# Kernel tuning notes

Measured on AMD Instinct MI355X. Metric: run time of the kernel, lower is better.

The kernel has to match this reference:

```python
import jax, jax.numpy as jnp
import numpy as np

N_NODES = 50000
N_EDGES = 1600000
IN_CH = 128
HID = 64
HEADS = 2
EMB = 128
OUT_CH = EMB // HEADS  # 64, GATConvMean out_channels
NEG_SLOPE = 0.2


def _gat_conv(x, src, dst, W, a_src, a_dst, b, heads, out_ch, concat, n_nodes):
    # x: [N, F_in]; W: [F_in, heads*out_ch]; a_src/a_dst: [heads, out_ch]; b: bias
    s = (x @ W).reshape(n_nodes, heads, out_ch)          # [N, H, C]
    alpha_src = jnp.sum(s * a_src, axis=-1)              # [N, H]
    alpha_dst = jnp.sum(s * a_dst, axis=-1)              # [N, H]
    e = jax.nn.leaky_relu(alpha_src[src] + alpha_dst[dst], NEG_SLOPE)  # [E, H]
    # segment softmax over edges sharing the same destination node
    m = jax.ops.segment_max(e, dst, num_segments=n_nodes)             # [N, H]
    ex = jnp.exp(e - m[dst])
    denom = jax.ops.segment_sum(ex, dst, num_segments=n_nodes)        # [N, H]
    alpha = ex / denom[dst]                                           # [E, H]
    msg = s[src] * alpha[:, :, None]                                  # [E, H, C]
    out = jax.ops.segment_sum(msg, dst, num_segments=n_nodes)         # [N, H, C]
    if concat:
        out = out.reshape(n_nodes, heads * out_ch)
    else:
        out = out.mean(axis=1)
    return out + b


def setup_inputs() -> dict:
    key = jax.random.key(0)
    ks = jax.random.split(key, 16)
    X = jax.random.normal(ks[0], (N_NODES, IN_CH), dtype=jnp.float32)
    edge_index = jax.random.randint(ks[1], (2, N_EDGES), 0, N_NODES, dtype=jnp.int64)

    def glorot(k, shape):
        fan_in, fan_out = shape[0], shape[-1]
        lim = jnp.sqrt(6.0 / (fan_in + fan_out)).astype(jnp.float32)
        return jax.random.uniform(k, shape, jnp.float32, -lim, lim)

    HC = HEADS * HID  # 128
    # in_layer: GATConv(IN_CH -> HID, heads=HEADS, concat)
    W0 = glorot(ks[2], (IN_CH, HC))
    a_src0 = glorot(ks[3], (HEADS, HID))
    a_dst0 = glorot(ks[4], (HEADS, HID))
    b0 = jnp.zeros((HC,), jnp.float32)
    # middle layer: GATConv(HC -> HID, heads=HEADS, concat)
    W1 = glorot(ks[5], (HC, HC))
    a_src1 = glorot(ks[6], (HEADS, HID))
    a_dst1 = glorot(ks[7], (HEADS, HID))
    b1 = jnp.zeros((HC,), jnp.float32)
    # ivectors: GATConvMean(HC -> OUT_CH, heads=HEADS, mean over heads)
    W2 = glorot(ks[8], (HC, HEADS * OUT_CH))
    a_src2 = glorot(ks[9], (HEADS, OUT_CH))
    a_dst2 = glorot(ks[10], (HEADS, OUT_CH))
    b2 = jnp.zeros((OUT_CH,), jnp.float32)
    return {
        "X": X, "edge_index": edge_index,
        "W0": W0, "a_src0": a_src0, "a_dst0": a_dst0, "b0": b0,
        "W1": W1, "a_src1": a_src1, "a_dst1": a_dst1, "b1": b1,
        "W2": W2, "a_src2": a_src2, "a_dst2": a_dst2, "b2": b2,
    }


def reference(X, edge_index, W0, a_src0, a_dst0, b0, W1, a_src1, a_dst1, b1, W2, a_src2, a_dst2, b2):
    n = X.shape[0]
    loop = jnp.arange(n, dtype=edge_index.dtype)
    src = jnp.concatenate([edge_index[0], loop])  # PyG GATConv add_self_loops=True
    dst = jnp.concatenate([edge_index[1], loop])
    h = jax.nn.elu(_gat_conv(X, src, dst, W0, a_src0, a_dst0, b0, HEADS, HID, True, n))
    h = jax.nn.relu(_gat_conv(h, src, dst, W1, a_src1, a_dst1, b1, HEADS, HID, True, n))
    # dropout is identity in eval mode
    out = jax.nn.relu(_gat_conv(h, src, dst, W2, a_src2, a_dst2, b2, HEADS, OUT_CH, False, n))
    return out
```

## Files before the change

### kernel.cpp

```cpp
#include <hip/hip_runtime.h>
#include <hip/hip_bf16.h>


#define SCAN_BLOCK 256

__global__ void detect_i64(const unsigned* __restrict__ ei, int* __restrict__ flag) {
    if (threadIdx.x == 0 && blockIdx.x == 0) {
        int allz = 1;
        for (int i = 0; i < 128; ++i)
            if (ei[2 * i + 1] != 0u) { allz = 0; break; }
        *flag = allz;
    }
}

__global__ __launch_bounds__(256) void gat_convert(
    const void* __restrict__ ei, const int* __restrict__ flag, int nE, int nN,
    int* __restrict__ srci, int* __restrict__ dsti) {
    const int i64 = *flag;
    const long long total = (long long)nE + nN;
    const long long stride = (long long)gridDim.x * blockDim.x;
    for (long long i = (long long)blockIdx.x * blockDim.x + threadIdx.x; i < total; i += stride) {
        int s, d;
        if (i < nE) {
            if (i64) { s = (int)((const long long*)ei)[i]; d = (int)((const long long*)ei)[nE + i]; }
            else     { s = ((const int*)ei)[i];            d = ((const int*)ei)[nE + i]; }
        } else { s = d = (int)(i - nE); }
        srci[i] = s;
        dsti[i] = d;
    }
}

__global__ __launch_bounds__(256) void gat_rankp(
    const int* __restrict__ dsti, long long total, int nN,
    int* __restrict__ cnt, int* __restrict__ rank) {
    const int cw = (nN + 7) >> 3;
    const int lo = (blockIdx.x & 7) * cw;
    const long long stride = (long long)(gridDim.x >> 3) * blockDim.x;
    for (long long i = (long long)(blockIdx.x >> 3) * blockDim.x + threadIdx.x;
         i < total; i += stride) {
        const int d = dsti[i];
        if ((unsigned)(d - lo) >= (unsigned)cw) continue;
        rank[i] = atomicAdd(&cnt[d], 1);
    }
}

__global__ __launch_bounds__(SCAN_BLOCK) void scan_stage1(
    const int* __restrict__ cnt, int* __restrict__ partial, int* __restrict__ bsum, int n) {
    __shared__ int tmp[SCAN_BLOCK];
    const int i = blockIdx.x * SCAN_BLOCK + threadIdx.x;
    const int v = (i < n) ? cnt[i] : 0;
    tmp[threadIdx.x] = v;
    __syncthreads();
    #pragma unroll
    for (int off = 1; off < SCAN_BLOCK; off <<= 1) {
        const int t = (threadIdx.x >= off) ? tmp[threadIdx.x - off] : 0;
        __syncthreads();
        tmp[threadIdx.x] += t;
        __syncthreads();
    }
    if (i < n) partial[i] = tmp[threadIdx.x];
    if (threadIdx.x == SCAN_BLOCK - 1) bsum[blockIdx.x] = tmp[threadIdx.x];
}

__global__ void scan_stage2(int* __restrict__ bsum, int nb, int* __restrict__ rowp, int n) {
    const int lane = threadIdx.x;
    int carry = 0;
    for (int base = 0; base < nb; base += 64) {
        const int i = base + lane;
        const int v = (i < nb) ? bsum[i] : 0;
        int incl = v;
        #pragma unroll
        for (int off = 1; off < 64; off <<= 1) {
            const int t = __shfl_up(incl, off);
            if (lane >= off) incl += t;
        }
        if (i < nb) bsum[i] = carry + incl - v;
        carry += __shfl(incl, 63);
    }
    if (lane == 0) rowp[n] = carry;
}

__global__ __launch_bounds__(SCAN_BLOCK) void scan_stage3(
    const int* __restrict__ partial, const int* __restrict__ cnt, const int* __restrict__ bsum,
    int* __restrict__ rowp, int n) {
    const int i = blockIdx.x * SCAN_BLOCK + threadIdx.x;
    if (i < n) rowp[i] = bsum[i >> 8] + partial[i] - cnt[i];
}

__global__ __launch_bounds__(256) void gat_placep(
    const int* __restrict__ srci, const int* __restrict__ dsti,
    const int* __restrict__ rank, const int* __restrict__ rowp,
    long long total, int nN, int* __restrict__ csr) {
    const int cw = (nN + 7) >> 3;
    const int lo = (blockIdx.x & 7) * cw;
    const long long stride = (long long)(gridDim.x >> 3) * blockDim.x;
    for (long long i = (long long)(blockIdx.x >> 3) * blockDim.x + threadIdx.x;
         i < total; i += stride) {
        const int d = dsti[i];
        if ((unsigned)(d - lo) >= (unsigned)cw) continue;
        csr[rowp[d] + rank[i]] = srci[i];
    }
}

__global__ __launch_bounds__(256) void gemm_alpha(
    const float* __restrict__ Xin, const float* __restrict__ W,
    const float* __restrict__ avs, const float* __restrict__ avd,
    float* __restrict__ S, float* __restrict__ as_, float* __restrict__ ad_, int n) {
    __shared__ float Xl[64][128];
    const int tid = threadIdx.x;
    const int row0 = blockIdx.x * 64;
    for (int i = tid; i < 64 * 32; i += 256) {
        const int r = i >> 5, c4 = i & 31;
        const int gr = row0 + r;
        float4 v = (gr < n) ? ((const float4*)(Xin + (size_t)gr * 128))[c4]
                            : make_float4(0.f, 0.f, 0.f, 0.f);
        ((float4*)(&Xl[r][0]))[c4] = v;
    }
    __syncthreads();
    const int col4 = tid & 31;
    const int rowg = tid >> 5;
    float4 acc[8];
    #pragma unroll
    for (int r = 0; r < 8; ++r) acc[r] = make_float4(0.f, 0.f, 0.f, 0.f);
    const float* Wc = W + col4 * 4;
    for (int kk = 0; kk < 128; kk += 4) {
        const float4 w0 = *(const float4*)(Wc + (size_t)(kk + 0) * 128);
        const float4 w1 = *(const float4*)(Wc + (size_t)(kk + 1) * 128);
        const float4 w2 = *(const float4*)(Wc + (size_t)(kk + 2) * 128);
        const float4 w3 = *(const float4*)(Wc + (size_t)(kk + 3) * 128);
        #pragma unroll
        for (int r = 0; r < 8; ++r) {
            const float4 x = *(const float4*)(&Xl[rowg * 8 + r][kk]);
            acc[r].x = fmaf(x.x, w0.x, acc[r].x); acc[r].y = fmaf(x.x, w0.y, acc[r].y);
            acc[r].z = fmaf(x.x, w0.z, acc[r].z); acc[r].w = fmaf(x.x, w0.w, acc[r].w);
            acc[r].x = fmaf(x.y, w1.x, acc[r].x); acc[r].y = fmaf(x.y, w1.y, acc[r].y);
            acc[r].z = fmaf(x.y, w1.z, acc[r].z); acc[r].w = fmaf(x.y, w1.w, acc[r].w);
            acc[r].x = fmaf(x.z, w2.x, acc[r].x); acc[r].y = fmaf(x.z, w2.y, acc[r].y);
            acc[r].z = fmaf(x.z, w2.z, acc[r].z); acc[r].w = fmaf(x.z, w2.w, acc[r].w);
            acc[r].x = fmaf(x.w, w3.x, acc[r].x); acc[r].y = fmaf(x.w, w3.y, acc[r].y);
            acc[r].z = fmaf(x.w, w3.z, acc[r].z); acc[r].w = fmaf(x.w, w3.w, acc[r].w);
        }
    }
    const float4 av = ((const float4*)avs)[col4];
    const float4 dv = ((const float4*)avd)[col4];
    #pragma unroll
    for (int r = 0; r < 8; ++r) {
        const int grow = row0 + rowg * 8 + r;
        if (grow < n) ((float4*)(S + (size_t)grow * 128))[col4] = acc[r];
        float ps = acc[r].x * av.x + acc[r].y * av.y + acc[r].z * av.z + acc[r].w * av.w;
        float pd = acc[r].x * dv.x + acc[r].y * dv.y + acc[r].z * dv.z + acc[r].w * dv.w;
        #pragma unroll
        for (int off = 8; off; off >>= 1) {
            ps += __shfl_xor(ps, off);
            pd += __shfl_xor(pd, off);
        }
        if ((col4 & 15) == 0 && grow < n) {
            const int h = col4 >> 4;
            as_[2 * grow + h] = ps;
            ad_[2 * grow + h] = pd;
        }
    }
}

__global__ __launch_bounds__(256) void gat_fused(
    const float* __restrict__ S, const float* __restrict__ as_,
    const float* __restrict__ ad_, const int* __restrict__ rowp,
    const int* __restrict__ csr, const float* __restrict__ bias,
    float* __restrict__ out, int n, int mode) {
    const int lane = threadIdx.x & 63;
    const int d = (blockIdx.x * blockDim.x + threadIdx.x) >> 6;
    if (d >= n) return;
    const int beg = rowp[d], end = rowp[d + 1];
    const int deg = end - beg;
    const float2 adv = *(const float2*)(ad_ + 2 * d);
    const int g = lane >> 4;
    const int gl = lane & 15;
    float4 acc0 = make_float4(0.f, 0.f, 0.f, 0.f);
    float4 acc1 = make_float4(0.f, 0.f, 0.f, 0.f);
    if (deg <= 64) {
        const bool has = lane < deg;
        const int s_reg = has ? csr[beg + lane] : 0;
        float e0 = -1e30f, e1 = -1e30f;
        if (has) {
            const float2 asv = *(const float2*)(as_ + 2 * s_reg);
            e0 = asv.x + adv.x; e0 = e0 > 0.f ? e0 : 0.2f * e0;
            e1 = asv.y + adv.y; e1 = e1 > 0.f ? e1 : 0.2f * e1;
        }
        float m0 = e0, m1 = e1;
        #pragma unroll
        for (int off = 32; off; off >>= 1) {
            m0 = fmaxf(m0, __shfl_xor(m0, off));
            m1 = fmaxf(m1, __shfl_xor(m1, off));
        }
        const float p0 = has ? __expf(e0 - m0) : 0.f;
        const float p1 = has ? __expf(e1 - m1) : 0.f;
        float s0 = p0, s1 = p1;
        #pragma unroll
        for (int off = 32; off; off >>= 1) {
            s0 += __shfl_xor(s0, off);
            s1 += __shfl_xor(s1, off);
        }
        const float inv0 = 1.f / s0, inv1 = 1.f / s1;
        int k = 0;
        for (; k + 4 <= deg; k += 4) {
            const int ke = k + g;
            const int sv = __shfl(s_reg, ke);
            const float a0 = __shfl(p0, ke) * inv0;
            const float a1 = __shfl(p1, ke) * inv1;
            const float4* r = (const float4*)(S + ((size_t)sv << 7));
            const float4 v0 = r[gl], v1 = r[16 + gl];
            acc0.x = fmaf(a0, v0.x, acc0.x); acc0.y = fmaf(a0, v0.y, acc0.y);
            acc0.z = fmaf(a0, v0.z, acc0.z); acc0.w = fmaf(a0, v0.w, acc0.w);
            acc1.x = fmaf(a1, v1.x, acc1.x); acc1.y = fmaf(a1, v1.y, acc1.y);
            acc1.z = fmaf(a1, v1.z, acc1.z); acc1.w = fmaf(a1, v1.w, acc1.w);
        }
        if (k < deg) {
            const int ke = k + g;
            const bool valid = ke < deg;
            const int idx = valid ? ke : 0;
            const int sv = __shfl(s_reg, idx);
            const float q0 = __shfl(p0, idx), q1 = __shfl(p1, idx);
            const float a0 = valid ? q0 * inv0 : 0.f;
            const float a1 = valid ? q1 * inv1 : 0.f;
            const float4* r = (const float4*)(S + ((size_t)sv << 7));
            const float4 v0 = r[gl], v1 = r[16 + gl];
            acc0.x = fmaf(a0, v0.x, acc0.x); acc0.y = fmaf(a0, v0.y, acc0.y);
            acc0.z = fmaf(a0, v0.z, acc0.z); acc0.w = fmaf(a0, v0.w, acc0.w);
            acc1.x = fmaf(a1, v1.x, acc1.x); acc1.y = fmaf(a1, v1.y, acc1.y);
            acc1.z = fmaf(a1, v1.z, acc1.z); acc1.w = fmaf(a1, v1.w, acc1.w);
        }
    } else {
        float m0 = -1e30f, m1 = -1e30f;
        for (int i = beg + lane; i < end; i += 64) {
            const int s = csr[i];
            const float2 asv = *(const float2*)(as_ + 2 * s);
            float e0 = asv.x + adv.x; e0 = e0 > 0.f ? e0 : 0.2f * e0;
            float e1 = asv.y + adv.y; e1 = e1 > 0.f ? e1 : 0.2f * e1;
            m0 = fmaxf(m0, e0); m1 = fmaxf(m1, e1);
        }
        #pragma unroll
        for (int off = 32; off; off >>= 1) {
            m0 = fmaxf(m0, __shfl_xor(m0, off));
            m1 = fmaxf(m1, __shfl_xor(m1, off));
        }
        float s0 = 0.f, s1 = 0.f;
        for (int i = beg + lane; i < end; i += 64) {
            const int s = csr[i];
            const float2 asv = *(const float2*)(as_ + 2 * s);
            float e0 = asv.x + adv.x; e0 = e0 > 0.f ? e0 : 0.2f * e0;
            float e1 = asv.y + adv.y; e1 = e1 > 0.f ? e1 : 0.2f * e1;
            s0 += __expf(e0 - m0); s1 += __expf(e1 - m1);
        }
        #pragma unroll
        for (int off = 32; off; off >>= 1) {
            s0 += __shfl_xor(s0, off);
            s1 += __shfl_xor(s1, off);
        }
        const float inv0 = 1.f / s0, inv1 = 1.f / s1;
        for (int k = 0; k < deg; k += 4) {
            const int ke = k + g;
            const bool valid = ke < deg;
            const int j = beg + (valid ? ke : 0);
            const int sv = csr[j];
            const float2 asv = *(const float2*)(as_ + 2 * sv);
            float e0 = asv.x + adv.x; e0 = e0 > 0.f ? e0 : 0.2f * e0;
            float e1 = asv.y + adv.y; e1 = e1 > 0.f ? e1 : 0.2f * e1;
            const float a0 = valid ? __expf(e0 - m0) * inv0 : 0.f;
            const float a1 = valid ? __expf(e1 - m1) * inv1 : 0.f;
            const float4* r = (const float4*)(S + ((size_t)sv << 7));
            const float4 v0 = r[gl], v1 = r[16 + gl];
            acc0.x = fmaf(a0, v0.x, acc0.x); acc0.y = fmaf(a0, v0.y, acc0.y);
            acc0.z = fmaf(a0, v0.z, acc0.z); acc0.w = fmaf(a0, v0.w, acc0.w);
            acc1.x = fmaf(a1, v1.x, acc1.x); acc1.y = fmaf(a1, v1.y, acc1.y);
            acc1.z = fmaf(a1, v1.z, acc1.z); acc1.w = fmaf(a1, v1.w, acc1.w);
        }
    }
    #pragma unroll
    for (int off = 16; off <= 32; off <<= 1) {
        acc0.x += __shfl_xor(acc0.x, off); acc0.y += __shfl_xor(acc0.y, off);
        acc0.z += __shfl_xor(acc0.z, off); acc0.w += __shfl_xor(acc0.w, off);
        acc1.x += __shfl_xor(acc1.x, off); acc1.y += __shfl_xor(acc1.y, off);
        acc1.z += __shfl_xor(acc1.z, off); acc1.w += __shfl_xor(acc1.w, off);
    }
    if (mode == 2) {
        if (lane < 16) {
            const float4 b = ((const float4*)bias)[gl];
            float4 o;
            o.x = fmaxf(0.5f * (acc0.x + acc1.x) + b.x, 0.f);
            o.y = fmaxf(0.5f * (acc0.y + acc1.y) + b.y, 0.f);
            o.z = fmaxf(0.5f * (acc0.z + acc1.z) + b.z, 0.f);
            o.w = fmaxf(0.5f * (acc0.w + acc1.w) + b.w, 0.f);
            ((float4*)(out + (size_t)d * 64))[gl] = o;
        }
    } else if (lane < 32) {
        const int ci = (lane < 16) ? gl : 16 + gl;
        const float4 a = (lane < 16) ? acc0 : acc1;
        const float4 b = ((const float4*)bias)[ci];
        float4 o;
        o.x = a.x + b.x; o.y = a.y + b.y; o.z = a.z + b.z; o.w = a.w + b.w;
        if (mode == 0) {
            o.x = o.x > 0.f ? o.x : expm1f(o.x);
            o.y = o.y > 0.f ? o.y : expm1f(o.y);
            o.z = o.z > 0.f ? o.z : expm1f(o.z);
            o.w = o.w > 0.f ? o.w : expm1f(o.w);
        } else {
            o.x = fmaxf(o.x, 0.f); o.y = fmaxf(o.y, 0.f);
            o.z = fmaxf(o.z, 0.f); o.w = fmaxf(o.w, 0.f);
        }
        ((float4*)(out + (size_t)d * 128))[ci] = o;
    }
}

extern "C" void kernel_launch(void* const* d_in, const int* in_sizes, int n_in,
                              void* d_out, int out_size, void* d_ws, size_t ws_size,
                              hipStream_t stream) {
    const float* X   = (const float*)d_in[0];
    const void*  EI  = d_in[1];
    const float* W0  = (const float*)d_in[2];
    const float* as0 = (const float*)d_in[3];
    const float* ad0 = (const float*)d_in[4];
    const float* b0  = (const float*)d_in[5];
    const float* W1  = (const float*)d_in[6];
    const float* as1 = (const float*)d_in[7];
    const float* ad1 = (const float*)d_in[8];
    const float* b1  = (const float*)d_in[9];
    const float* W2  = (const float*)d_in[10];
    const float* as2 = (const float*)d_in[11];
    const float* ad2 = (const float*)d_in[12];
    const float* b2  = (const float*)d_in[13];

    const int N  = in_sizes[0] / 128;
    const int E  = in_sizes[1] / 2;
    const int ET = E + N;
    const int NB = (N + SCAN_BLOCK - 1) / SCAN_BLOCK;

    char* p = (char*)d_ws;
    size_t used = 0;
    auto alloc = [&](size_t bytes) -> void* {
        void* r = p + used;
        used += (bytes + 255) & ~(size_t)255;
        return r;
    };
    float*  S    = (float*)alloc((size_t)N * 128 * 4);
    float*  H0   = (float*)alloc((size_t)N * 128 * 4);
    float*  H1   = (float*)alloc((size_t)N * 128 * 4);
    int*    csr  = (int*)alloc((size_t)ET * 4);
    int*    rowp = (int*)alloc((size_t)(N + 1) * 4);
    int*    cnt  = (int*)alloc((size_t)N * 4);
    int*    part = (int*)alloc((size_t)N * 4);
    int*    bsum = (int*)alloc((size_t)NB * 4);
    float*  asb  = (float*)alloc((size_t)N * 2 * 4);
    float*  adb  = (float*)alloc((size_t)N * 2 * 4);
    int*    flag = (int*)alloc(256);
    if (used > ws_size) return;
    const int ETP = (ET + 63) & ~63;
    int* srci = (int*)S;
    int* dsti = srci + ETP;
    int* rank = dsti + ETP;

    hipMemsetAsync(cnt, 0, (size_t)N * 4, stream);
    detect_i64<<<1, 64, 0, stream>>>((const unsigned*)EI, flag);
    gat_convert<<<2048, 256, 0, stream>>>(EI, flag, E, N, srci, dsti);
    gat_rankp<<<2048, 256, 0, stream>>>(dsti, (long long)ET, N, cnt, rank);
    scan_stage1<<<NB, SCAN_BLOCK, 0, stream>>>(cnt, part, bsum, N);
    scan_stage2<<<1, 64, 0, stream>>>(bsum, NB, rowp, N);
    scan_stage3<<<NB, SCAN_BLOCK, 0, stream>>>(part, cnt, bsum, rowp, N);
    gat_placep<<<2048, 256, 0, stream>>>(srci, dsti, rank, rowp, (long long)ET, N, csr);

    const int gemm_blocks = (N + 63) / 64;
    const int wave_blocks = (N + 3) / 4;

    gemm_alpha<<<gemm_blocks, 256, 0, stream>>>(X, W0, as0, ad0, S, asb, adb, N);
    gat_fused<<<wave_blocks, 256, 0, stream>>>(S, asb, adb, rowp, csr, b0, H0, N, 0);
    gemm_alpha<<<gemm_blocks, 256, 0, stream>>>(H0, W1, as1, ad1, S, asb, adb, N);
    gat_fused<<<wave_blocks, 256, 0, stream>>>(S, asb, adb, rowp, csr, b1, H1, N, 1);
    gemm_alpha<<<gemm_blocks, 256, 0, stream>>>(H1, W2, as2, ad2, S, asb, adb, N);
    gat_fused<<<wave_blocks, 256, 0, stream>>>(S, asb, adb, rowp, csr, b2, (float*)d_out, N, 2);
}
```

Baseline: 547.1 us.

## Sort CSR neighbors by source-range bins to improve gather locality

Each edge is binned by destination and coarse source block (src>>12, 13 bins per node). The CSR is built over these finer bins with a two-level scan, so each node's neighbor list is roughly ordered by source index. Edges are also packed as int2, and the tail loops skip the loads for invalid lanes. The aim is better L2 locality for the S-row gathers in the three aggregation passes. The cost is a 13x larger count, scan and memset array (650k bins) and an extra scan level.

```diff
diff --git a/kernel.cpp b/kernel.cpp
--- a/kernel.cpp
+++ b/kernel.cpp
@@ -3,6 +3,8 @@
 
 
 #define SCAN_BLOCK 256
+#define KSHIFT 12
+#define KC 13
 
 __global__ void detect_i64(const unsigned* __restrict__ ei, int* __restrict__ flag) {
     if (threadIdx.x == 0 && blockIdx.x == 0) {
@@ -15,7 +17,7 @@
 
 __global__ __launch_bounds__(256) void gat_convert(
     const void* __restrict__ ei, const int* __restrict__ flag, int nE, int nN,
-    int* __restrict__ srci, int* __restrict__ dsti) {
+    int2* __restrict__ edge2) {
     const int i64 = *flag;
     const long long total = (long long)nE + nN;
     const long long stride = (long long)gridDim.x * blockDim.x;
@@ -25,22 +27,22 @@
             if (i64) { s = (int)((const long long*)ei)[i]; d = (int)((const long long*)ei)[nE + i]; }
             else     { s = ((const int*)ei)[i];            d = ((const int*)ei)[nE + i]; }
         } else { s = d = (int)(i - nE); }
-        srci[i] = s;
-        dsti[i] = d;
+        edge2[i] = make_int2(s, d);
     }
 }
 
 __global__ __launch_bounds__(256) void gat_rankp(
-    const int* __restrict__ dsti, long long total, int nN,
-    int* __restrict__ cnt, int* __restrict__ rank) {
+    const int2* __restrict__ edge2, long long total, int nN,
+    int* __restrict__ cnt2, int* __restrict__ rank) {
     const int cw = (nN + 7) >> 3;
     const int lo = (blockIdx.x & 7) * cw;
     const long long stride = (long long)(gridDim.x >> 3) * blockDim.x;
     for (long long i = (long long)(blockIdx.x >> 3) * blockDim.x + threadIdx.x;
          i < total; i += stride) {
-        const int d = dsti[i];
-        if ((unsigned)(d - lo) >= (unsigned)cw) continue;
-        rank[i] = atomicAdd(&cnt[d], 1);
+        const int2 e = edge2[i];
+        if ((unsigned)(e.y - lo) >= (unsigned)cw) continue;
+        const int bin = e.y * KC + (e.x >> KSHIFT);
+        rank[i] = atomicAdd(&cnt2[bin], 1);
     }
 }
 
@@ -80,25 +82,29 @@
     if (lane == 0) rowp[n] = carry;
 }
 
-__global__ __launch_bounds__(SCAN_BLOCK) void scan_stage3(
-    const int* __restrict__ partial, const int* __restrict__ cnt, const int* __restrict__ bsum,
-    int* __restrict__ rowp, int n) {
+__global__ __launch_bounds__(SCAN_BLOCK) void scan_stage3v2(
+    const int* __restrict__ part2, const int* __restrict__ cnt2,
+    const int* __restrict__ bsumA, const int* __restrict__ partB,
+    const int* __restrict__ bsumB, int* __restrict__ rowp, int n) {
     const int i = blockIdx.x * SCAN_BLOCK + threadIdx.x;
-    if (i < n) rowp[i] = bsum[i >> 8] + partial[i] - cnt[i];
+    if (i < n) {
+        const int b1 = i >> 8;
+        rowp[i] = bsumB[b1 >> 8] + (partB[b1] - bsumA[b1]) + (part2[i] - cnt2[i]);
+    }
 }
 
 __global__ __launch_bounds__(256) void gat_placep(
-    const int* __restrict__ srci, const int* __restrict__ dsti,
-    const int* __restrict__ rank, const int* __restrict__ rowp,
-    long long total, int nN, int* __restrict__ csr) {
+    const int2* __restrict__ edge2, const int* __restrict__ rank,
+    const int* __restrict__ rowp2, long long total, int nN, int* __restrict__ csr) {
     const int cw = (nN + 7) >> 3;
     const int lo = (blockIdx.x & 7) * cw;
     const long long stride = (long long)(gridDim.x >> 3) * blockDim.x;
     for (long long i = (long long)(blockIdx.x >> 3) * blockDim.x + threadIdx.x;
          i < total; i += stride) {
-        const int d = dsti[i];
-        if ((unsigned)(d - lo) >= (unsigned)cw) continue;
-        csr[rowp[d] + rank[i]] = srci[i];
+        const int2 e = edge2[i];
+        if ((unsigned)(e.y - lo) >= (unsigned)cw) continue;
+        const int bin = e.y * KC + (e.x >> KSHIFT);
+        csr[rowp2[bin] + rank[i]] = e.x;
     }
 }
 
@@ -164,13 +170,13 @@
 
 __global__ __launch_bounds__(256) void gat_fused(
     const float* __restrict__ S, const float* __restrict__ as_,
-    const float* __restrict__ ad_, const int* __restrict__ rowp,
+    const float* __restrict__ ad_, const int* __restrict__ rowp2,
     const int* __restrict__ csr, const float* __restrict__ bias,
     float* __restrict__ out, int n, int mode) {
     const int lane = threadIdx.x & 63;
     const int d = (blockIdx.x * blockDim.x + threadIdx.x) >> 6;
     if (d >= n) return;
-    const int beg = rowp[d], end = rowp[d + 1];
+    const int beg = rowp2[d * KC], end = rowp2[(d + 1) * KC];
     const int deg = end - beg;
     const float2 adv = *(const float2*)(ad_ + 2 * d);
     const int g = lane >> 4;
@@ -220,14 +226,15 @@
             const int idx = valid ? ke : 0;
             const int sv = __shfl(s_reg, idx);
             const float q0 = __shfl(p0, idx), q1 = __shfl(p1, idx);
-            const float a0 = valid ? q0 * inv0 : 0.f;
-            const float a1 = valid ? q1 * inv1 : 0.f;
-            const float4* r = (const float4*)(S + ((size_t)sv << 7));
-            const float4 v0 = r[gl], v1 = r[16 + gl];
-            acc0.x = fmaf(a0, v0.x, acc0.x); acc0.y = fmaf(a0, v0.y, acc0.y);
-            acc0.z = fmaf(a0, v0.z, acc0.z); acc0.w = fmaf(a0, v0.w, acc0.w);
-            acc1.x = fmaf(a1, v1.x, acc1.x); acc1.y = fmaf(a1, v1.y, acc1.y);
-            acc1.z = fmaf(a1, v1.z, acc1.z); acc1.w = fmaf(a1, v1.w, acc1.w);
+            if (valid) {
+                const float a0 = q0 * inv0, a1 = q1 * inv1;
+                const float4* r = (const float4*)(S + ((size_t)sv << 7));
+                const float4 v0 = r[gl], v1 = r[16 + gl];
+                acc0.x = fmaf(a0, v0.x, acc0.x); acc0.y = fmaf(a0, v0.y, acc0.y);
+                acc0.z = fmaf(a0, v0.z, acc0.z); acc0.w = fmaf(a0, v0.w, acc0.w);
+                acc1.x = fmaf(a1, v1.x, acc1.x); acc1.y = fmaf(a1, v1.y, acc1.y);
+                acc1.z = fmaf(a1, v1.z, acc1.z); acc1.w = fmaf(a1, v1.w, acc1.w);
+            }
         }
     } else {
         float m0 = -1e30f, m1 = -1e30f;
@@ -260,19 +267,20 @@
         for (int k = 0; k < deg; k += 4) {
             const int ke = k + g;
             const bool valid = ke < deg;
-            const int j = beg + (valid ? ke : 0);
-            const int sv = csr[j];
-            const float2 asv = *(const float2*)(as_ + 2 * sv);
-            float e0 = asv.x + adv.x; e0 = e0 > 0.f ? e0 : 0.2f * e0;
-            float e1 = asv.y + adv.y; e1 = e1 > 0.f ? e1 : 0.2f * e1;
-            const float a0 = valid ? __expf(e0 - m0) * inv0 : 0.f;
-            const float a1 = valid ? __expf(e1 - m1) * inv1 : 0.f;
-            const float4* r = (const float4*)(S + ((size_t)sv << 7));
-            const float4 v0 = r[gl], v1 = r[16 + gl];
-            acc0.x = fmaf(a0, v0.x, acc0.x); acc0.y = fmaf(a0, v0.y, acc0.y);
-            acc0.z = fmaf(a0, v0.z, acc0.z); acc0.w = fmaf(a0, v0.w, acc0.w);
-            acc1.x = fmaf(a1, v1.x, acc1.x); acc1.y = fmaf(a1, v1.y, acc1.y);
-            acc1.z = fmaf(a1, v1.z, acc1.z); acc1.w = fmaf(a1, v1.w, acc1.w);
+            if (valid) {
+                const int sv = csr[beg + ke];
+                const float2 asv = *(const float2*)(as_ + 2 * sv);
+                float e0 = asv.x + adv.x; e0 = e0 > 0.f ? e0 : 0.2f * e0;
+                float e1 = asv.y + adv.y; e1 = e1 > 0.f ? e1 : 0.2f * e1;
+                const float a0 = __expf(e0 - m0) * inv0;
+                const float a1 = __expf(e1 - m1) * inv1;
+                const float4* r = (const float4*)(S + ((size_t)sv << 7));
+                const float4 v0 = r[gl], v1 = r[16 + gl];
+                acc0.x = fmaf(a0, v0.x, acc0.x); acc0.y = fmaf(a0, v0.y, acc0.y);
+                acc0.z = fmaf(a0, v0.z, acc0.z); acc0.w = fmaf(a0, v0.w, acc0.w);
+                acc1.x = fmaf(a1, v1.x, acc1.x); acc1.y = fmaf(a1, v1.y, acc1.y);
+                acc1.z = fmaf(a1, v1.z, acc1.z); acc1.w = fmaf(a1, v1.w, acc1.w);
+            }
         }
     }
     #pragma unroll
@@ -332,7 +340,9 @@
     const int N  = in_sizes[0] / 128;
     const int E  = in_sizes[1] / 2;
     const int ET = E + N;
-    const int NB = (N + SCAN_BLOCK - 1) / SCAN_BLOCK;
+    const int NBINS = N * KC;
+    const int NB2 = (NBINS + SCAN_BLOCK - 1) / SCAN_BLOCK;
+    const int NB3 = (NB2 + SCAN_BLOCK - 1) / SCAN_BLOCK;
 
     char* p = (char*)d_ws;
     size_t used = 0;
@@ -341,39 +351,41 @@
         used += (bytes + 255) & ~(size_t)255;
         return r;
     };
-    float*  S    = (float*)alloc((size_t)N * 128 * 4);
-    float*  H0   = (float*)alloc((size_t)N * 128 * 4);
-    float*  H1   = (float*)alloc((size_t)N * 128 * 4);
-    int*    csr  = (int*)alloc((size_t)ET * 4);
-    int*    rowp = (int*)alloc((size_t)(N + 1) * 4);
-    int*    cnt  = (int*)alloc((size_t)N * 4);
-    int*    part = (int*)alloc((size_t)N * 4);
-    int*    bsum = (int*)alloc((size_t)NB * 4);
-    float*  asb  = (float*)alloc((size_t)N * 2 * 4);
-    float*  adb  = (float*)alloc((size_t)N * 2 * 4);
-    int*    flag = (int*)alloc(256);
+    float*  S     = (float*)alloc((size_t)N * 128 * 4);
+    float*  H0    = (float*)alloc((size_t)N * 128 * 4);
+    float*  H1    = (float*)alloc((size_t)N * 128 * 4);
+    int*    csr   = (int*)alloc((size_t)ET * 4);
+    int*    rowp2 = (int*)alloc((size_t)(NBINS + 1) * 4);
+    int*    cnt2  = (int*)alloc((size_t)NBINS * 4);
+    int*    part2 = (int*)alloc((size_t)NBINS * 4);
+    int*    bsumA = (int*)alloc((size_t)NB2 * 4);
+    int*    partB = (int*)alloc((size_t)NB2 * 4);
+    int*    bsumB = (int*)alloc((size_t)NB3 * 4);
+    float*  asb   = (float*)alloc((size_t)N * 2 * 4);
+    float*  adb   = (float*)alloc((size_t)N * 2 * 4);
+    int*    flag  = (int*)alloc(256);
     if (used > ws_size) return;
     const int ETP = (ET + 63) & ~63;
-    int* srci = (int*)S;
-    int* dsti = srci + ETP;
-    int* rank = dsti + ETP;
-
-    hipMemsetAsync(cnt, 0, (size_t)N * 4, stream);
+    int2* edge2 = (int2*)S;
+    int*  rank  = (int*)(edge2 + ETP);
+
+    hipMemsetAsync(cnt2, 0, (size_t)NBINS * 4, stream);
     detect_i64<<<1, 64, 0, stream>>>((const unsigned*)EI, flag);
-    gat_convert<<<2048, 256, 0, stream>>>(EI, flag, E, N, srci, dsti);
-    gat_rankp<<<2048, 256, 0, stream>>>(dsti, (long long)ET, N, cnt, rank);
-    scan_stage1<<<NB, SCAN_BLOCK, 0, stream>>>(cnt, part, bsum, N);
-    scan_stage2<<<1, 64, 0, stream>>>(bsum, NB, rowp, N);
-    scan_stage3<<<NB, SCAN_BLOCK, 0, stream>>>(part, cnt, bsum, rowp, N);
-    gat_placep<<<2048, 256, 0, stream>>>(srci, dsti, rank, rowp, (long long)ET, N, csr);
+    gat_convert<<<2048, 256, 0, stream>>>(EI, flag, E, N, edge2);
+    gat_rankp<<<2048, 256, 0, stream>>>(edge2, (long long)ET, N, cnt2, rank);
+    scan_stage1<<<NB2, SCAN_BLOCK, 0, stream>>>(cnt2, part2, bsumA, NBINS);
+    scan_stage1<<<NB3, SCAN_BLOCK, 0, stream>>>(bsumA, partB, bsumB, NB2);
+    scan_stage2<<<1, 64, 0, stream>>>(bsumB, NB3, rowp2, NBINS);
+    scan_stage3v2<<<NB2, SCAN_BLOCK, 0, stream>>>(part2, cnt2, bsumA, partB, bsumB, rowp2, NBINS);
+    gat_placep<<<2048, 256, 0, stream>>>(edge2, rank, rowp2, (long long)ET, N, csr);
 
     const int gemm_blocks = (N + 63) / 64;
     const int wave_blocks = (N + 3) / 4;
 
     gemm_alpha<<<gemm_blocks, 256, 0, stream>>>(X, W0, as0, ad0, S, asb, adb, N);
-    gat_fused<<<wave_blocks, 256, 0, stream>>>(S, asb, adb, rowp, csr, b0, H0, N, 0);
+    gat_fused<<<wave_blocks, 256, 0, stream>>>(S, asb, adb, rowp2, csr, b0, H0, N, 0);
     gemm_alpha<<<gemm_blocks, 256, 0, stream>>>(H0, W1, as1, ad1, S, asb, adb, N);
-    gat_fused<<<wave_blocks, 256, 0, stream>>>(S, asb, adb, rowp, csr, b1, H1, N, 1);
+    gat_fused<<<wave_blocks, 256, 0, stream>>>(S, asb, adb, rowp2, csr, b1, H1, N, 1);
     gemm_alpha<<<gemm_blocks, 256, 0, stream>>>(H1, W2, as2, ad2, S, asb, adb, N);
-    gat_fused<<<wave_blocks, 256, 0, stream>>>(S, asb, adb, rowp, csr, b2, (float*)d_out, N, 2);
-}
+    gat_fused<<<wave_blocks, 256, 0, stream>>>(S, asb, adb, rowp2, csr, b2, (float*)d_out, N, 2);
+}
```

After: 535.0 us. 1.02x faster.
